# Optimization experiments

Measured on AMD Instinct MI355X. Metric: run time of the kernel, lower is better.

The kernel has to match this reference:

```python
import jax, jax.numpy as jnp
import numpy as np

EMBED_DIM = 512
NUM_HEADS = 8
HEAD_DIM = EMBED_DIM // NUM_HEADS
K_NEIGH = 3
SEQ_N = 16384
BATCH = 4


def setup_inputs() -> dict:
    key = jax.random.key(0)
    ks = jax.random.split(key, 12)
    x = jax.random.normal(ks[0], (BATCH, SEQ_N, EMBED_DIM), dtype=jnp.float32)
    neighbor_table = jax.random.randint(ks[1], (K_NEIGH, SEQ_N), 0, SEQ_N, dtype=jnp.int64)
    s = 0.02
    Wq = jax.random.normal(ks[2], (EMBED_DIM, EMBED_DIM), jnp.float32) * s
    bq = jnp.zeros((EMBED_DIM,), jnp.float32)
    Wk = jax.random.normal(ks[3], (EMBED_DIM, EMBED_DIM), jnp.float32) * s
    bk = jnp.zeros((EMBED_DIM,), jnp.float32)
    Wv = jax.random.normal(ks[4], (EMBED_DIM, EMBED_DIM), jnp.float32) * s
    bv = jnp.zeros((EMBED_DIM,), jnp.float32)
    Wo = jax.random.normal(ks[5], (EMBED_DIM, EMBED_DIM), jnp.float32) * s
    bo = jnp.zeros((EMBED_DIM,), jnp.float32)
    return {"x": x, "neighbor_table": neighbor_table,
            "Wq": Wq, "bq": bq, "Wk": Wk, "bk": bk,
            "Wv": Wv, "bv": bv, "Wo": Wo, "bo": bo}


def reference(x, neighbor_table, Wq, bq, Wk, bk, Wv, bv, Wo, bo):
    B, N, C = x.shape
    H, d = NUM_HEADS, HEAD_DIM
    scale = d ** (-0.5)
    # buffers derived from neighbor_table (matches module __init__)
    valid = (neighbor_table != -1)                      # (K, N)
    idx = jnp.clip(neighbor_table, 0)                   # (K, N)

    # projections; nn.Linear: y = x @ W.T + b
    def proj(W, b):
        return (jnp.einsum('bnc,oc->bno', x, W) + b).reshape(B, N, H, d).transpose(0, 2, 1, 3)  # (B,H,N,d)

    q = proj(Wq, bq)
    k = proj(Wk, bk)
    v = proj(Wv, bv)

    # gather neighbors: (B, H, K, N, d)
    k_nb = k[:, :, idx, :]
    v_nb = v[:, :, idx, :]

    # scores over head_dim: (B, H, K, N)
    scores = jnp.einsum('bhnd,bhknd->bhkn', q, k_nb) * scale
    scores = jnp.where(valid[None, None], scores, -jnp.inf)
    attn = jax.nn.softmax(scores, axis=2)               # softmax over K neighbors
    # dropout is identity (eval / p used only at train)

    out = jnp.einsum('bhkn,bhknd->bhnd', attn, v_nb)    # (B,H,N,d)
    out = out.transpose(0, 2, 1, 3).reshape(B, N, C)
    out = jnp.einsum('bnc,oc->bno', out, Wo) + bo
    return out
```

## Files before the change

### kernel.cpp

```cpp
#include <hip/hip_runtime.h>
#include <stdint.h>

#define SEQN 16384
#define NBATCH 4

typedef __attribute__((ext_vector_type(8))) __bf16 bf16x8;
typedef __attribute__((ext_vector_type(4))) float f32x4;
typedef __attribute__((ext_vector_type(4))) unsigned int u32x4;

__device__ __forceinline__ unsigned int f2bf(float f) {
  unsigned int x = __builtin_bit_cast(unsigned int, f);
  x = x + 0x7fffu + ((x >> 16) & 1u);
  return x >> 16;
}
__device__ __forceinline__ float bf2f(unsigned int lo) {
  return __builtin_bit_cast(float, lo << 16);
}

__device__ __forceinline__ void gload_lds16(const unsigned short* g, unsigned char* l) {
  __builtin_amdgcn_global_load_lds(
      (const __attribute__((address_space(1))) unsigned int*)g,
      (__attribute__((address_space(3))) unsigned int*)l, 16, 0, 0);
}

template<bool OUT_BF16>
__global__ __launch_bounds__(256, 2)
void gemm_bt(const unsigned short* __restrict__ A,
             const unsigned short* __restrict__ Bt,
             const float* __restrict__ bias,
             void* __restrict__ Cout,
             int Ncols, int K)
{
  __shared__ __align__(16) unsigned char lA[128 * 64 * 2];
  __shared__ __align__(16) unsigned char lB[128 * 64 * 2];
  const int tid = threadIdx.x;
  const int lane = tid & 63;
  const int wid = tid >> 6;
  const int wr = (wid >> 1) * 64;
  const int wc = (wid & 1) * 64;
  const int nbx = Ncols >> 7;
  const int bx = (int)blockIdx.x % nbx;
  const int by = (int)blockIdx.x / nbx;
  const long row0 = (long)by << 7;
  const int col0 = bx << 7;

  f32x4 acc[4][4];
#pragma unroll
  for (int i = 0; i < 4; ++i)
#pragma unroll
    for (int j = 0; j < 4; ++j) acc[i][j] = (f32x4)0.0f;

  for (int kt = 0; kt < K; kt += 64) {
#pragma unroll
    for (int i = 0; i < 4; ++i) {
      const int f = i * 256 + tid;
      const int r = f >> 3;
      const int cd = (f & 7) ^ (r & 7);
      gload_lds16(A + (row0 + r) * (long)K + kt + cd * 8, lA + f * 16);
      gload_lds16(Bt + (long)(col0 + r) * K + kt + cd * 8, lB + f * 16);
    }
    __syncthreads();
#pragma unroll
    for (int kk = 0; kk < 2; ++kk) {
      bf16x8 af[4], bfv[4];
#pragma unroll
      for (int fm = 0; fm < 4; ++fm) {
        const int row = wr + fm * 16 + (lane & 15);
        const int ch = (kk * 4 + (lane >> 4)) ^ (row & 7);
        af[fm] = __builtin_bit_cast(bf16x8, *(const u32x4*)(lA + row * 128 + ch * 16));
      }
#pragma unroll
      for (int fn = 0; fn < 4; ++fn) {
        const int row = wc + fn * 16 + (lane & 15);
        const int ch = (kk * 4 + (lane >> 4)) ^ (row & 7);
        bfv[fn] = __builtin_bit_cast(bf16x8, *(const u32x4*)(lB + row * 128 + ch * 16));
      }
#pragma unroll
      for (int fm = 0; fm < 4; ++fm)
#pragma unroll
        for (int fn = 0; fn < 4; ++fn)
          acc[fm][fn] = __builtin_amdgcn_mfma_f32_16x16x32_bf16(af[fm], bfv[fn], acc[fm][fn], 0, 0, 0);
    }
    __syncthreads();
  }

#pragma unroll
  for (int fn = 0; fn < 4; ++fn) {
    const int n = col0 + wc + fn * 16 + (lane & 15);
    const float bn = bias[n];
#pragma unroll
    for (int fm = 0; fm < 4; ++fm) {
      const long mbase = row0 + wr + fm * 16 + ((lane >> 4) << 2);
#pragma unroll
      for (int j = 0; j < 4; ++j) {
        const float v = acc[fm][fn][j] + bn;
        if constexpr (OUT_BF16)
          ((unsigned short*)Cout)[(mbase + j) * (long)Ncols + n] = (unsigned short)f2bf(v);
        else
          ((float*)Cout)[(mbase + j) * (long)Ncols + n] = v;
      }
    }
  }
}

__global__ __launch_bounds__(256)
void nbr_attn(const unsigned short* __restrict__ qkv,
              const int* __restrict__ nbr,
              unsigned short* __restrict__ aout)
{
  const int wid = (int)((blockIdx.x * 256 + threadIdx.x) >> 6);
  const int lane = threadIdx.x & 63;
  const int n = wid & (SEQN - 1);
  const int b = wid >> 14;

  const unsigned short* qrow = qkv + (size_t)wid * 1536;
  float qv[8];
  {
    const u32x4 raw = *(const u32x4*)(qrow + lane * 8);
#pragma unroll
    for (int i = 0; i < 4; ++i) {
      qv[2 * i] = bf2f(raw[i] & 0xffffu);
      qv[2 * i + 1] = bf2f(raw[i] >> 16);
    }
  }
  float s[3];
  u32x4 vraw[3];
  bool val[3];
#pragma unroll
  for (int k = 0; k < 3; ++k) {
    const int t = nbr[k * SEQN + n];
    val[k] = (t != -1);
    const int j = t > 0 ? t : 0;
    const unsigned short* krow = qkv + ((size_t)(b * SEQN + j)) * 1536 + 512;
    const u32x4 kraw = *(const u32x4*)(krow + lane * 8);
    vraw[k] = *(const u32x4*)(krow + 512 + lane * 8);
    float d = 0.f;
#pragma unroll
    for (int i = 0; i < 4; ++i)
      d += qv[2 * i] * bf2f(kraw[i] & 0xffffu) + qv[2 * i + 1] * bf2f(kraw[i] >> 16);
    d += __shfl_xor(d, 1);
    d += __shfl_xor(d, 2);
    d += __shfl_xor(d, 4);
    s[k] = d * 0.125f;
  }
  float m = -3.0e38f;
#pragma unroll
  for (int k = 0; k < 3; ++k)
    if (val[k]) m = fmaxf(m, s[k]);
  float e[3], sum = 0.f;
#pragma unroll
  for (int k = 0; k < 3; ++k) {
    e[k] = val[k] ? __expf(s[k] - m) : 0.f;
    sum += e[k];
  }
  const float inv = sum > 0.f ? 1.f / sum : 0.f;
  float acc[8] = {0.f, 0.f, 0.f, 0.f, 0.f, 0.f, 0.f, 0.f};
#pragma unroll
  for (int k = 0; k < 3; ++k) {
    const float w = e[k] * inv;
#pragma unroll
    for (int i = 0; i < 4; ++i) {
      acc[2 * i] += w * bf2f(vraw[k][i] & 0xffffu);
      acc[2 * i + 1] += w * bf2f(vraw[k][i] >> 16);
    }
  }
  u32x4 o;
#pragma unroll
  for (int i = 0; i < 4; ++i)
    o[i] = f2bf(acc[2 * i]) | (f2bf(acc[2 * i + 1]) << 16);
  *(u32x4*)(aout + (size_t)wid * 512 + lane * 8) = o;
}

__global__ __launch_bounds__(256)
void cvt_f32_bf16(const float* __restrict__ in, unsigned short* __restrict__ out, int n8) {
  int i = blockIdx.x * 256 + threadIdx.x;
  const int stride = gridDim.x * 256;
  for (; i < n8; i += stride) {
    const float4* p = (const float4*)(in + (size_t)i * 8);
    const float4 a = p[0], c = p[1];
    u32x4 o;
    o[0] = f2bf(a.x) | (f2bf(a.y) << 16);
    o[1] = f2bf(a.z) | (f2bf(a.w) << 16);
    o[2] = f2bf(c.x) | (f2bf(c.y) << 16);
    o[3] = f2bf(c.z) | (f2bf(c.w) << 16);
    *(u32x4*)(out + (size_t)i * 8) = o;
  }
}

__global__ __launch_bounds__(256)
void prep_w(const float* __restrict__ Wq, const float* __restrict__ Wk,
            const float* __restrict__ Wv, const float* __restrict__ Wo,
            const float* __restrict__ bq, const float* __restrict__ bk,
            const float* __restrict__ bv,
            unsigned short* __restrict__ wf, unsigned short* __restrict__ wo,
            float* __restrict__ biasf)
{
  const int i = blockIdx.x * 256 + threadIdx.x;
  const int stride = gridDim.x * 256;
  for (int t = i; t < 262144; t += stride) {
    wf[t] = (unsigned short)f2bf(Wq[t]);
    wf[262144 + t] = (unsigned short)f2bf(Wk[t]);
    wf[524288 + t] = (unsigned short)f2bf(Wv[t]);
    wo[t] = (unsigned short)f2bf(Wo[t]);
  }
  if (i < 512) {
    biasf[i] = bq[i];
    biasf[512 + i] = bk[i];
    biasf[1024 + i] = bv[i];
  }
}

extern "C" void kernel_launch(void* const* d_in, const int* in_sizes, int n_in,
                              void* d_out, int out_size, void* d_ws, size_t ws_size,
                              hipStream_t stream) {
  const float* x  = (const float*)d_in[0];
  const int* nbr  = (const int*)d_in[1];
  const float* Wq = (const float*)d_in[2];
  const float* bq = (const float*)d_in[3];
  const float* Wk = (const float*)d_in[4];
  const float* bk = (const float*)d_in[5];
  const float* Wv = (const float*)d_in[6];
  const float* bv = (const float*)d_in[7];
  const float* Wo = (const float*)d_in[8];
  const float* bo = (const float*)d_in[9];
  float* out = (float*)d_out;
  unsigned char* ws = (unsigned char*)d_ws;

  unsigned short* xb  = (unsigned short*)(ws);
  unsigned short* qkv = (unsigned short*)(ws + 67108864UL);
  unsigned short* wf  = (unsigned short*)(ws + 268435456UL);
  unsigned short* wo  = (unsigned short*)(ws + 270008320UL);
  float* biasf        = (float*)(ws + 270532608UL);

  cvt_f32_bf16<<<4096, 256, 0, stream>>>(x, xb, 33554432 / 8);
  prep_w<<<1024, 256, 0, stream>>>(Wq, Wk, Wv, Wo, bq, bk, bv, wf, wo, biasf);
  gemm_bt<true><<<dim3(512 * 12), 256, 0, stream>>>(xb, wf, biasf, qkv, 1536, 512);
  nbr_attn<<<16384, 256, 0, stream>>>(qkv, nbr, xb);
  gemm_bt<false><<<dim3(512 * 4), 256, 0, stream>>>(xb, wo, bo, out, 512, 512);
}
```

Baseline: 298.5 us.

## Swizzle GEMM block order, raise occupancy bound, hoist neighbor loads in attention

The GEMM now remaps block indices in groups of 8 so that concurrently running blocks share A rows and B columns in cache. Its launch bounds ask for 4 blocks per SIMD instead of 2, which may tighten the register budget and cause spills. In the neighbor-attention kernel, all neighbor indices and K/V rows are loaded up front, before any compute. This lets the gather latencies overlap rather than being serialized through the dot-product loop.

Result: faster. 284.3 us (-4.7%).

```diff
diff --git a/kernel.cpp b/kernel.cpp
--- a/kernel.cpp
+++ b/kernel.cpp
@@ -24,7 +24,7 @@
 }
 
 template<bool OUT_BF16>
-__global__ __launch_bounds__(256, 2)
+__global__ __launch_bounds__(256, 4)
 void gemm_bt(const unsigned short* __restrict__ A,
              const unsigned short* __restrict__ Bt,
              const float* __restrict__ bias,
@@ -39,8 +39,11 @@
   const int wr = (wid >> 1) * 64;
   const int wc = (wid & 1) * 64;
   const int nbx = Ncols >> 7;
-  const int bx = (int)blockIdx.x % nbx;
-  const int by = (int)blockIdx.x / nbx;
+  const int bid = (int)blockIdx.x;
+  const int cpx = (int)gridDim.x >> 3;
+  const int swz = (bid & 7) * cpx + (bid >> 3);
+  const int bx = swz % nbx;
+  const int by = swz / nbx;
   const long row0 = (long)by << 7;
   const int col0 = bx << 7;
 
@@ -114,30 +117,37 @@
   const int b = wid >> 14;
 
   const unsigned short* qrow = qkv + (size_t)wid * 1536;
+  const u32x4 qraw = *(const u32x4*)(qrow + lane * 8);
+
+  int t0 = nbr[n];
+  int t1 = nbr[SEQN + n];
+  int t2 = nbr[2 * SEQN + n];
+  bool val[3] = {t0 != -1, t1 != -1, t2 != -1};
+  const unsigned short* base = qkv + (size_t)b * SEQN * 1536 + 512 + lane * 8;
+  const unsigned short* k0 = base + (size_t)(t0 > 0 ? t0 : 0) * 1536;
+  const unsigned short* k1 = base + (size_t)(t1 > 0 ? t1 : 0) * 1536;
+  const unsigned short* k2 = base + (size_t)(t2 > 0 ? t2 : 0) * 1536;
+  u32x4 kraw[3], vraw[3];
+  kraw[0] = *(const u32x4*)k0;
+  vraw[0] = *(const u32x4*)(k0 + 512);
+  kraw[1] = *(const u32x4*)k1;
+  vraw[1] = *(const u32x4*)(k1 + 512);
+  kraw[2] = *(const u32x4*)k2;
+  vraw[2] = *(const u32x4*)(k2 + 512);
+
   float qv[8];
-  {
-    const u32x4 raw = *(const u32x4*)(qrow + lane * 8);
-#pragma unroll
-    for (int i = 0; i < 4; ++i) {
-      qv[2 * i] = bf2f(raw[i] & 0xffffu);
-      qv[2 * i + 1] = bf2f(raw[i] >> 16);
-    }
+#pragma unroll
+  for (int i = 0; i < 4; ++i) {
+    qv[2 * i] = bf2f(qraw[i] & 0xffffu);
+    qv[2 * i + 1] = bf2f(qraw[i] >> 16);
   }
   float s[3];
-  u32x4 vraw[3];
-  bool val[3];
 #pragma unroll
   for (int k = 0; k < 3; ++k) {
-    const int t = nbr[k * SEQN + n];
-    val[k] = (t != -1);
-    const int j = t > 0 ? t : 0;
-    const unsigned short* krow = qkv + ((size_t)(b * SEQN + j)) * 1536 + 512;
-    const u32x4 kraw = *(const u32x4*)(krow + lane * 8);
-    vraw[k] = *(const u32x4*)(krow + 512 + lane * 8);
     float d = 0.f;
 #pragma unroll
     for (int i = 0; i < 4; ++i)
-      d += qv[2 * i] * bf2f(kraw[i] & 0xffffu) + qv[2 * i + 1] * bf2f(kraw[i] >> 16);
+      d += qv[2 * i] * bf2f(kraw[k][i] & 0xffffu) + qv[2 * i + 1] * bf2f(kraw[k][i] >> 16);
     d += __shfl_xor(d, 1);
     d += __shfl_xor(d, 2);
     d += __shfl_xor(d, 4);
```
